# Optimization experiments

Measured on AMD Instinct MI355X. Metric: run time of the kernel, lower is better.

## Reference

```python
import jax, jax.numpy as jnp
import numpy as np

BLOCK_SIZE = 64
NUM_STEPS = 3
# pad_type='post', init_type='ones', attention_mask=None


def setup_inputs() -> dict:
    key = jax.random.key(0)
    k1, k2, k3 = jax.random.split(key, 3)
    B, H, S, D = 4, 16, 4096, 64
    return {
        "query": jax.random.normal(k1, (B, H, S, D), dtype=jnp.float32),
        "key": jax.random.normal(k2, (B, H, S, D), dtype=jnp.float32),
        "value": jax.random.normal(k3, (B, H, S, D), dtype=jnp.float32),
    }


def _soba_monarch(query, key, value):
    B, H, S, D = query.shape
    bs = BLOCK_SIZE
    nb = -(-S // bs)                 # ceil(S / bs)
    pad = nb * bs - S                # post padding amount
    q = query / (D ** 0.5)

    pad_cfg = ((0, 0), (0, 0), (0, pad), (0, 0))
    Qb = jnp.pad(q, pad_cfg).reshape(B, H, nb, bs, D)      # (l j) v -> l j v
    Kb = jnp.pad(key, pad_cfg).reshape(B, H, nb, bs, D)    # (k i) v -> k i v

    # validity of positions in the padded sequence (post-pad)
    pos_valid = (jnp.arange(nb * bs) < S).reshape(nb, bs)  # [block, within]
    # left factor shape (..., j, l, k): rows of the flattened (l j) axis
    left_mask = jnp.broadcast_to(pos_valid.T[:, :, None], (bs, nb, nb))      # j l k
    # right factor shape (..., k, j, i): columns of the flattened (k i) axis
    right_mask = jnp.broadcast_to(pos_valid[:, None, :], (nb, bs, bs))       # k j i

    NEG = jnp.finfo(q.dtype).min
    # init_type = 'ones'
    left = jnp.broadcast_to(
        jnp.where(left_mask, 1.0 / nb, 0.0), (B, H, bs, nb, nb)
    ).astype(q.dtype)

    for _ in range(NUM_STEPS):
        # beta[k,j,i] = sum_{l,v} left[j,l,k] Q[l,j,v] K[k,i,v]
        beta = jnp.einsum('bhjlk,bhljv,bhkiv->bhkji', left, Qb, Kb, optimize=True)
        tau = jnp.swapaxes(jnp.sum(left, axis=-2), -1, -2)[..., None]        # bhkj1
        tau_zero = jnp.isclose(tau, 0.0)
        tau_safe = jnp.where(tau_zero, 1.0, tau)
        logits_r = jnp.where(right_mask & ~tau_zero, beta / tau_safe, NEG)
        right = jax.nn.softmax(logits_r, axis=-1)
        right = jnp.where(right_mask, right, 0.0)

        # alpha[j,1,k] = sum_i right[k,j,i] log right[k,j,i]  (xlogy)
        r_safe = jnp.where(right > 0, right, 1.0)
        alpha = jnp.sum(right * jnp.log(r_safe), axis=-1)                    # bhkj
        alpha = jnp.swapaxes(alpha, -1, -2)[..., None, :]                    # bhj1k

        beta2 = jnp.einsum('bhkji,bhljv,bhkiv->bhjlk', right, Qb, Kb, optimize=True)
        left = jax.nn.softmax(jnp.where(left_mask, beta2 - alpha, NEG), axis=-1)
        left = jnp.where(left_mask, left, 0.0)

    # multiply: z = L (R V)
    Vb = jnp.pad(value, pad_cfg).reshape(B, H, nb, bs, D)                    # k i v
    Y = jnp.einsum('bhkji,bhkiv->bhkjv', right, Vb)
    Z = jnp.einsum('bhjlk,bhkjv->bhljv', left, Y)
    z = Z.reshape(B, H, nb * bs, D)
    return z[..., :S, :]


def reference(query, key, value):
    return _soba_monarch(query, key, value)
```

## Files before the change

### kernel.cpp

```cpp
#include <hip/hip_runtime.h>


namespace {

typedef __attribute__((ext_vector_type(8))) short short8v;
typedef __attribute__((ext_vector_type(4))) float f32x4;

constexpr int HEADS = 64;
constexpr size_t HEADQ = 262144;
constexpr size_t MATF  = (size_t)HEADS * 262144;

#define MFMA(ACC, A, B) ACC = __builtin_amdgcn_mfma_f32_16x16x32_bf16(A, B, ACC, 0, 0, 0)
#define LD8(arr, row, g8) (*(const short8v*)((arr) + (row) * 72 + (g8) * 8))

__device__ __forceinline__ float rmax16(float m) {
    m = fmaxf(m, __shfl_xor(m, 1));
    m = fmaxf(m, __shfl_xor(m, 2));
    m = fmaxf(m, __shfl_xor(m, 4));
    m = fmaxf(m, __shfl_xor(m, 8));
    return m;
}
__device__ __forceinline__ float rsum16(float s) {
    s += __shfl_xor(s, 1);
    s += __shfl_xor(s, 2);
    s += __shfl_xor(s, 4);
    s += __shfl_xor(s, 8);
    return s;
}

__device__ __forceinline__ void bfsplit(float x, ushort& h, ushort& l) {
    uint u = __float_as_uint(x);
    uint hi = (u + 0x7FFFu + ((u >> 16) & 1u)) & 0xFFFF0000u;
    h = (ushort)(hi >> 16);
    l = (ushort)(__float_as_uint(x - __uint_as_float(hi)) >> 16);
}
__device__ __forceinline__ uint packbf(float x) {
    uint u = __float_as_uint(x);
    uint hi = (u + 0x7FFFu + ((u >> 16) & 1u)) & 0xFFFF0000u;
    return hi | (__float_as_uint(x - __uint_as_float(hi)) >> 16);
}

struct Frag16 { short8v h0, h1, l0, l1; };

__device__ __forceinline__ Frag16 load_packed16(const uint* p) {
    Frag16 f;
    #pragma unroll
    for (int q = 0; q < 4; ++q) {
        uint4 a = *(const uint4*)(p + 4 * q);
        uint vv[4] = {a.x, a.y, a.z, a.w};
        #pragma unroll
        for (int e = 0; e < 4; ++e) {
            const int i = 4 * q + e;
            const ushort hh = (ushort)(vv[e] >> 16), ll = (ushort)(vv[e] & 0xFFFFu);
            if (i < 8) { f.h0[i] = (short)hh; f.l0[i] = (short)ll; }
            else       { f.h1[i - 8] = (short)hh; f.l1[i - 8] = (short)ll; }
        }
    }
    return f;
}
__device__ __forceinline__ Frag16 load_f32x16(const float* p, float s) {
    Frag16 f;
    #pragma unroll
    for (int q = 0; q < 4; ++q) {
        float4 a = *(const float4*)(p + 4 * q);
        float vv[4] = {a.x * s, a.y * s, a.z * s, a.w * s};
        #pragma unroll
        for (int e = 0; e < 4; ++e) {
            const int i = 4 * q + e;
            ushort hh, ll; bfsplit(vv[e], hh, ll);
            if (i < 8) { f.h0[i] = (short)hh; f.l0[i] = (short)ll; }
            else       { f.h1[i - 8] = (short)hh; f.l1[i - 8] = (short)ll; }
        }
    }
    return f;
}
__device__ __forceinline__ void store_rows(ushort* H, ushort* L, int r, int c0,
                                           const Frag16& f) {
    *(short8v*)(H + r * 72 + c0)     = f.h0;
    *(short8v*)(H + r * 72 + c0 + 8) = f.h1;
    *(short8v*)(L + r * 72 + c0)     = f.l0;
    *(short8v*)(L + r * 72 + c0 + 8) = f.l1;
}
__device__ __forceinline__ void scatter_tr(ushort* H, ushort* L, int r, int c0,
                                           const Frag16& f) {
    #pragma unroll
    for (int e = 0; e < 8; ++e) {
        H[(c0 + e) * 72 + r] = (ushort)f.h0[e];
        L[(c0 + e) * 72 + r] = (ushort)f.l0[e];
    }
    #pragma unroll
    for (int e = 0; e < 8; ++e) {
        H[(c0 + 8 + e) * 72 + r] = (ushort)f.h1[e];
        L[(c0 + 8 + e) * 72 + r] = (ushort)f.l1[e];
    }
}

__device__ __forceinline__ void flush_u32(const uint* OS, uint* g, int tid) {
    #pragma unroll
    for (int q = 0; q < 4; ++q) {
        const int off = tid * 4 + q * 1024;
        uint4 v = *(const uint4*)(OS + (off >> 6) * 68 + (off & 63));
        *(uint4*)(g + off) = v;
    }
}

__device__ __forceinline__ void mmstep(const ushort* AH, const ushort* AL,
                                       const ushort* BH, const ushort* BL,
                                       int w, int lo4, int hi4, f32x4 acc[4]) {
    #pragma unroll
    for (int ks = 0; ks < 2; ++ks) {
        short8v ah = LD8(AH, 16 * w + lo4, hi4 + 4 * ks);
        short8v al = LD8(AL, 16 * w + lo4, hi4 + 4 * ks);
        #pragma unroll
        for (int t = 0; t < 4; ++t) {
            short8v bh = LD8(BH, 16 * t + lo4, hi4 + 4 * ks);
            short8v bl = LD8(BL, 16 * t + lo4, hi4 + 4 * ks);
            MFMA(acc[t], ah, bh); MFMA(acc[t], ah, bl); MFMA(acc[t], al, bh);
        }
    }
}

__global__ void kmean_kernel(const float* __restrict__ Q, uint* __restrict__ M) {
    const int wg = blockIdx.x;
    const int h  = wg >> 6, j = wg & 63;
    const int v  = threadIdx.x;
    const float* base = Q + (size_t)h * HEADQ + (size_t)j * 64 + v;
    float acc = 0.f;
    #pragma unroll
    for (int l = 0; l < 64; ++l) acc += base[(size_t)l * 4096];
    M[(size_t)wg * 64 + v] = packbf(acc * (1.0f / 512.0f));
}

template<int FIRST, int LAST>
__global__ __launch_bounds__(256) void bc_kernel(
    const uint*  __restrict__ Gsrc,
    const float* __restrict__ Kmat,
    const float* __restrict__ Vmat,
    const float* __restrict__ tauIn,
    uint*  __restrict__ HmOut,
    float* __restrict__ alphaOut,
    uint*  __restrict__ Yout)
{
    __shared__ uint SM[9216];
    ushort* Ah = (ushort*)SM;        ushort* Al = Ah + 4608;
    ushort* Bh = (ushort*)(SM + 4608); ushort* Bl = Bh + 4608;
    uint* OS  = SM + 4608;
    uint* OS2 = SM;

    const int wg = blockIdx.x, h = wg >> 6, k = wg & 63;
    const int tid = threadIdx.x, r = tid & 63, c0 = (tid >> 6) << 4;

    {
        const uint* gp = FIRST ? (Gsrc + ((size_t)h * 64 + r) * 64 + c0)
                               : (Gsrc + ((size_t)h * 64 + r) * 4096 + (size_t)k * 64 + c0);
        Frag16 fg = load_packed16(gp);
        store_rows(Ah, Al, r, c0, fg);
    }
    Frag16 fk = load_f32x16(Kmat + (size_t)h * HEADQ + (size_t)k * 4096 + r * 64 + c0, 1.f);
    store_rows(Bh, Bl, r, c0, fk);
    Frag16 fv;
    if (LAST)
        fv = load_f32x16(Vmat + (size_t)h * HEADQ + (size_t)k * 4096 + r * 64 + c0, 1.f);

    const int w = tid >> 6, lo4 = tid & 15, hi4 = (tid >> 4) & 3;
    float tvv[4];
    #pragma unroll
    for (int rr = 0; rr < 4; ++rr)
        tvv[rr] = FIRST ? 1.f : tauIn[((size_t)h * 64 + k) * 64 + 16 * w + 4 * hi4 + rr];
    __syncthreads();

    f32x4 acc[4] = {};
    mmstep(Ah, Al, Bh, Bl, w, lo4, hi4, acc);
    __syncthreads();

    #pragma unroll
    for (int rr = 0; rr < 4; ++rr) {
        const int j = 16 * w + 4 * hi4 + rr;
        const bool tz = !(tvv[rr] > 1e-8f);
        const float tvi = tz ? 1.f : 1.f / tvv[rr];
        float lg[4];
        #pragma unroll
        for (int t = 0; t < 4; ++t) lg[t] = acc[t][rr] * tvi;
        float m = rmax16(fmaxf(fmaxf(lg[0], lg[1]), fmaxf(lg[2], lg[3])));
        float e[4], s = 0.f;
        #pragma unroll
        for (int t = 0; t < 4; ++t) { e[t] = __expf(lg[t] - m); s += e[t]; }
        s = rsum16(s);
        const float inv = 1.f / s;
        float ap = 0.f;
        #pragma unroll
        for (int t = 0; t < 4; ++t) {
            const float rv = tz ? (1.f / 64.f) : e[t] * inv;
            ap += (rv > 0.f) ? rv * __logf(rv) : 0.f;
            ushort hh, ll; bfsplit(rv, hh, ll);
            Ah[j * 72 + 16 * t + lo4] = hh;
            Al[j * 72 + 16 * t + lo4] = ll;
        }
        ap = rsum16(ap);
        if (lo4 == 0) alphaOut[((size_t)h * 64 + j) * 64 + k] = ap;
    }
    scatter_tr(Bh, Bl, r, c0, fk);
    __syncthreads();

    f32x4 acc2[4] = {};
    mmstep(Ah, Al, Bh, Bl, w, lo4, hi4, acc2);
    f32x4 acc3[4] = {};
    if (LAST) {
        __syncthreads();
        scatter_tr(Bh, Bl, r, c0, fv);
        __syncthreads();
        mmstep(Ah, Al, Bh, Bl, w, lo4, hi4, acc3);
    }
    __syncthreads();

    #pragma unroll
    for (int rr = 0; rr < 4; ++rr) {
        const int j = 16 * w + 4 * hi4 + rr;
        #pragma unroll
        for (int t = 0; t < 4; ++t) OS[j * 68 + 16 * t + lo4] = packbf(acc2[t][rr]);
    }
    if (LAST) {
        #pragma unroll
        for (int rr = 0; rr < 4; ++rr) {
            const int j = 16 * w + 4 * hi4 + rr;
            #pragma unroll
            for (int t = 0; t < 4; ++t) OS2[j * 68 + 16 * t + lo4] = packbf(acc3[t][rr]);
        }
    }
    __syncthreads();
    flush_u32(OS, HmOut + (size_t)wg * 4096, tid);
    if (LAST) flush_u32(OS2, Yout + (size_t)wg * 4096, tid);
}

template<int LAST>
__global__ __launch_bounds__(256) void da_kernel(
    const float* __restrict__ Q,
    const uint*  __restrict__ HmIn,
    const float* __restrict__ alphaIn,
    const uint*  __restrict__ Yin,
    uint*  __restrict__ Gout,
    float* __restrict__ tauOut,
    float* __restrict__ Zout)
{
    __shared__ uint SM[9216];
    ushort* Ah = (ushort*)SM;        ushort* Al = Ah + 4608;
    ushort* Bh = (ushort*)(SM + 4608); ushort* Bl = Bh + 4608;
    uint*  OSu = SM + 4608;
    float* OSf = (float*)(SM + 4608);

    const int wg = blockIdx.x, h = wg >> 6, j = wg & 63;
    const int tid = threadIdx.x, r = tid & 63, c0 = (tid >> 6) << 4;

    Frag16 fq = load_f32x16(Q + (size_t)h * HEADQ + (size_t)r * 4096 + (size_t)j * 64 + c0,
                            0.125f);
    store_rows(Ah, Al, r, c0, fq);
    {
        Frag16 fh = load_packed16(HmIn + ((size_t)h * 64 + r) * 4096 + (size_t)j * 64 + c0);
        store_rows(Bh, Bl, r, c0, fh);
    }
    Frag16 fy;
    if (LAST)
        fy = load_packed16(Yin + ((size_t)h * 64 + r) * 4096 + (size_t)j * 64 + c0);

    const int w = tid >> 6, lo4 = tid & 15, hi4 = (tid >> 4) & 3;
    float av[4];
    #pragma unroll
    for (int t = 0; t < 4; ++t)
        av[t] = alphaIn[((size_t)h * 64 + j) * 64 + 16 * t + lo4];
    __syncthreads();

    f32x4 acc[4] = {};
    mmstep(Ah, Al, Bh, Bl, w, lo4, hi4, acc);
    __syncthreads();

    #pragma unroll
    for (int rr = 0; rr < 4; ++rr) {
        const int l = 16 * w + 4 * hi4 + rr;
        float lg[4];
        #pragma unroll
        for (int t = 0; t < 4; ++t) lg[t] = acc[t][rr] - av[t];
        float m = rmax16(fmaxf(fmaxf(lg[0], lg[1]), fmaxf(lg[2], lg[3])));
        float e[4], s = 0.f;
        #pragma unroll
        for (int t = 0; t < 4; ++t) { e[t] = __expf(lg[t] - m); s += e[t]; }
        s = rsum16(s);
        const float inv = 1.f / s;
        #pragma unroll
        for (int t = 0; t < 4; ++t) {
            const float lv = e[t] * inv;
            ushort hh, ll; bfsplit(lv, hh, ll);
            if (!LAST) { Bh[(16 * t + lo4) * 72 + l] = hh; Bl[(16 * t + lo4) * 72 + l] = ll; }
            else       { Bh[l * 72 + 16 * t + lo4] = hh; Bl[l * 72 + 16 * t + lo4] = ll; }
        }
    }
    if (!LAST) scatter_tr(Ah, Al, r, c0, fq);
    else       scatter_tr(Ah, Al, r, c0, fy);
    __syncthreads();

    if (!LAST) {
        f32x4 acc2[4] = {};
        f32x4 tacc = {};
        short8v onesb;
        #pragma unroll
        for (int e2 = 0; e2 < 8; ++e2) onesb[e2] = (lo4 == 0) ? (short)0x3F80 : (short)0;
        #pragma unroll
        for (int ks = 0; ks < 2; ++ks) {
            short8v ah = LD8(Bh, 16 * w + lo4, hi4 + 4 * ks);
            short8v al = LD8(Bl, 16 * w + lo4, hi4 + 4 * ks);
            MFMA(tacc, ah, onesb); MFMA(tacc, al, onesb);
            #pragma unroll
            for (int t = 0; t < 4; ++t) {
                short8v bh = LD8(Ah, 16 * t + lo4, hi4 + 4 * ks);
                short8v bl = LD8(Al, 16 * t + lo4, hi4 + 4 * ks);
                MFMA(acc2[t], ah, bh); MFMA(acc2[t], ah, bl); MFMA(acc2[t], al, bh);
            }
        }
        __syncthreads();
        #pragma unroll
        for (int rr = 0; rr < 4; ++rr) {
            const int kq = 16 * w + 4 * hi4 + rr;
            if (lo4 == 0) tauOut[((size_t)h * 64 + kq) * 64 + j] = tacc[rr];
            #pragma unroll
            for (int t = 0; t < 4; ++t) OSu[kq * 68 + 16 * t + lo4] = packbf(acc2[t][rr]);
        }
        __syncthreads();
        flush_u32(OSu, Gout + (size_t)wg * 4096, tid);
    } else {
        f32x4 acc2[4] = {};
        #pragma unroll
        for (int ks = 0; ks < 2; ++ks) {
            short8v ah = LD8(Bh, 16 * w + lo4, hi4 + 4 * ks);
            short8v al = LD8(Bl, 16 * w + lo4, hi4 + 4 * ks);
            #pragma unroll
            for (int t = 0; t < 4; ++t) {
                short8v bh = LD8(Ah, 16 * t + lo4, hi4 + 4 * ks);
                short8v bl = LD8(Al, 16 * t + lo4, hi4 + 4 * ks);
                MFMA(acc2[t], ah, bh); MFMA(acc2[t], ah, bl); MFMA(acc2[t], al, bh);
            }
        }
        __syncthreads();
        #pragma unroll
        for (int rr = 0; rr < 4; ++rr) {
            const int l = 16 * w + 4 * hi4 + rr;
            #pragma unroll
            for (int t = 0; t < 4; ++t) OSf[l * 68 + 16 * t + lo4] = acc2[t][rr];
        }
        __syncthreads();
        #pragma unroll
        for (int q = 0; q < 4; ++q) {
            const int l = (tid >> 4) + 16 * q;
            const int v4 = (tid & 15) * 4;
            float4 vv = *(const float4*)(OSf + l * 68 + v4);
            *(float4*)(Zout + (size_t)h * HEADQ + (size_t)l * 4096 + (size_t)j * 64 + v4) = vv;
        }
    }
}

}

extern "C" void kernel_launch(void* const* d_in, const int* in_sizes, int n_in,
                              void* d_out, int out_size, void* d_ws, size_t ws_size,
                              hipStream_t stream) {
    const float* Q = (const float*)d_in[0];
    const float* K = (const float*)d_in[1];
    const float* V = (const float*)d_in[2];
    float* out = (float*)d_out;

    char* ws = (char*)d_ws;
    const size_t MB = 1024 * 1024;
    uint*  G   = (uint*)(ws);
    uint*  Hm  = (uint*)(ws + 64 * MB);
    uint*  M   = (uint*)(ws + 128 * MB);
    float* al  = (float*)(ws + 129 * MB);
    float* tau = (float*)(ws + 130 * MB);

    const bool bigws = ws_size >= (size_t)196 * MB;
    uint*  Ybuf = bigws ? (uint*)(ws + 131 * MB) : (uint*)out;
    float* Zdst = bigws ? out : (float*)G;

    dim3 blk(256), grid(HEADS * 64);

    kmean_kernel<<<dim3(HEADS * 64), dim3(64), 0, stream>>>(Q, M);
    bc_kernel<1, 0><<<grid, blk, 0, stream>>>(M, K, nullptr, nullptr, Hm, al, nullptr);
    da_kernel<0>   <<<grid, blk, 0, stream>>>(Q, Hm, al, nullptr, G, tau, nullptr);
    bc_kernel<0, 0><<<grid, blk, 0, stream>>>(G, K, nullptr, tau, Hm, al, nullptr);
    da_kernel<0>   <<<grid, blk, 0, stream>>>(Q, Hm, al, nullptr, G, tau, nullptr);
    bc_kernel<0, 1><<<grid, blk, 0, stream>>>(G, K, V, tau, Hm, al, Ybuf);
    da_kernel<1>   <<<grid, blk, 0, stream>>>(Q, Hm, al, Ybuf, nullptr, nullptr, Zdst);
    if (!bigws)
        hipMemcpyAsync(d_out, G, MATF * sizeof(float), hipMemcpyDeviceToDevice, stream);
}
```

Measured before the change: 305.5 us.

## Process four blocks per workgroup with register prefetch and fp32 intermediates

Measured after the change: 409.8 us. +34.1%, slower.

```diff
diff --git a/kernel.cpp b/kernel.cpp
--- a/kernel.cpp
+++ b/kernel.cpp
@@ -34,43 +34,27 @@
     h = (ushort)(hi >> 16);
     l = (ushort)(__float_as_uint(x - __uint_as_float(hi)) >> 16);
 }
-__device__ __forceinline__ uint packbf(float x) {
-    uint u = __float_as_uint(x);
-    uint hi = (u + 0x7FFFu + ((u >> 16) & 1u)) & 0xFFFF0000u;
-    return hi | (__float_as_uint(x - __uint_as_float(hi)) >> 16);
-}
-
+
+struct Raw16  { float4 a, b, c, d; };
 struct Frag16 { short8v h0, h1, l0, l1; };
 
-__device__ __forceinline__ Frag16 load_packed16(const uint* p) {
+__device__ __forceinline__ Raw16 raw_load(const float* p) {
+    Raw16 r;
+    r.a = *(const float4*)(p);
+    r.b = *(const float4*)(p + 4);
+    r.c = *(const float4*)(p + 8);
+    r.d = *(const float4*)(p + 12);
+    return r;
+}
+__device__ __forceinline__ Frag16 split16(const Raw16& r, float s) {
+    float v[16] = {r.a.x*s, r.a.y*s, r.a.z*s, r.a.w*s, r.b.x*s, r.b.y*s, r.b.z*s, r.b.w*s,
+                   r.c.x*s, r.c.y*s, r.c.z*s, r.c.w*s, r.d.x*s, r.d.y*s, r.d.z*s, r.d.w*s};
     Frag16 f;
     #pragma unroll
-    for (int q = 0; q < 4; ++q) {
-        uint4 a = *(const uint4*)(p + 4 * q);
-        uint vv[4] = {a.x, a.y, a.z, a.w};
-        #pragma unroll
-        for (int e = 0; e < 4; ++e) {
-            const int i = 4 * q + e;
-            const ushort hh = (ushort)(vv[e] >> 16), ll = (ushort)(vv[e] & 0xFFFFu);
-            if (i < 8) { f.h0[i] = (short)hh; f.l0[i] = (short)ll; }
-            else       { f.h1[i - 8] = (short)hh; f.l1[i - 8] = (short)ll; }
-        }
-    }
-    return f;
-}
-__device__ __forceinline__ Frag16 load_f32x16(const float* p, float s) {
-    Frag16 f;
-    #pragma unroll
-    for (int q = 0; q < 4; ++q) {
-        float4 a = *(const float4*)(p + 4 * q);
-        float vv[4] = {a.x * s, a.y * s, a.z * s, a.w * s};
-        #pragma unroll
-        for (int e = 0; e < 4; ++e) {
-            const int i = 4 * q + e;
-            ushort hh, ll; bfsplit(vv[e], hh, ll);
-            if (i < 8) { f.h0[i] = (short)hh; f.l0[i] = (short)ll; }
-            else       { f.h1[i - 8] = (short)hh; f.l1[i - 8] = (short)ll; }
-        }
+    for (int e = 0; e < 16; ++e) {
+        ushort hh, ll; bfsplit(v[e], hh, ll);
+        if (e < 8) { f.h0[e] = (short)hh; f.l0[e] = (short)ll; }
+        else       { f.h1[e - 8] = (short)hh; f.l1[e - 8] = (short)ll; }
     }
     return f;
 }
@@ -95,12 +79,12 @@
     }
 }
 
-__device__ __forceinline__ void flush_u32(const uint* OS, uint* g, int tid) {
+__device__ __forceinline__ void flush_f32(const float* OS, float* g, int tid) {
     #pragma unroll
     for (int q = 0; q < 4; ++q) {
         const int off = tid * 4 + q * 1024;
-        uint4 v = *(const uint4*)(OS + (off >> 6) * 68 + (off & 63));
-        *(uint4*)(g + off) = v;
+        float4 v = *(const float4*)(OS + (off >> 6) * 68 + (off & 63));
+        *(float4*)(g + off) = v;
     }
 }
 
@@ -120,239 +104,251 @@
     }
 }
 
-__global__ void kmean_kernel(const float* __restrict__ Q, uint* __restrict__ M) {
+__global__ __launch_bounds__(256) void kmean_kernel(const float* __restrict__ Q,
+                                                    float* __restrict__ M) {
     const int wg = blockIdx.x;
-    const int h  = wg >> 6, j = wg & 63;
-    const int v  = threadIdx.x;
+    const int h  = wg >> 4;
+    const int j  = ((wg & 15) << 2) + (threadIdx.x >> 6);
+    const int v  = threadIdx.x & 63;
     const float* base = Q + (size_t)h * HEADQ + (size_t)j * 64 + v;
     float acc = 0.f;
     #pragma unroll
     for (int l = 0; l < 64; ++l) acc += base[(size_t)l * 4096];
-    M[(size_t)wg * 64 + v] = packbf(acc * (1.0f / 512.0f));
+    M[((size_t)h * 64 + j) * 64 + v] = acc * (1.0f / 512.0f);
 }
 
 template<int FIRST, int LAST>
-__global__ __launch_bounds__(256) void bc_kernel(
-    const uint*  __restrict__ Gsrc,
+__global__ __launch_bounds__(256, 4) void bc_kernel(
+    const float* __restrict__ Gsrc,
     const float* __restrict__ Kmat,
     const float* __restrict__ Vmat,
     const float* __restrict__ tauIn,
-    uint*  __restrict__ HmOut,
+    float* __restrict__ HmOut,
     float* __restrict__ alphaOut,
-    uint*  __restrict__ Yout)
+    float* __restrict__ Yout)
 {
     __shared__ uint SM[9216];
-    ushort* Ah = (ushort*)SM;        ushort* Al = Ah + 4608;
+    ushort* Ah = (ushort*)SM;          ushort* Al = Ah + 4608;
     ushort* Bh = (ushort*)(SM + 4608); ushort* Bl = Bh + 4608;
-    uint* OS  = SM + 4608;
-    uint* OS2 = SM;
-
-    const int wg = blockIdx.x, h = wg >> 6, k = wg & 63;
+    float* OSB = (float*)(SM + 4608);
+    float* OSA = (float*)SM;
+
+    const int wg = blockIdx.x, h = wg >> 4, k0 = (wg & 15) << 2;
     const int tid = threadIdx.x, r = tid & 63, c0 = (tid >> 6) << 4;
-
-    {
-        const uint* gp = FIRST ? (Gsrc + ((size_t)h * 64 + r) * 64 + c0)
-                               : (Gsrc + ((size_t)h * 64 + r) * 4096 + (size_t)k * 64 + c0);
-        Frag16 fg = load_packed16(gp);
-        store_rows(Ah, Al, r, c0, fg);
-    }
-    Frag16 fk = load_f32x16(Kmat + (size_t)h * HEADQ + (size_t)k * 4096 + r * 64 + c0, 1.f);
-    store_rows(Bh, Bl, r, c0, fk);
-    Frag16 fv;
-    if (LAST)
-        fv = load_f32x16(Vmat + (size_t)h * HEADQ + (size_t)k * 4096 + r * 64 + c0, 1.f);
-
     const int w = tid >> 6, lo4 = tid & 15, hi4 = (tid >> 4) & 3;
-    float tvv[4];
-    #pragma unroll
-    for (int rr = 0; rr < 4; ++rr)
-        tvv[rr] = FIRST ? 1.f : tauIn[((size_t)h * 64 + k) * 64 + 16 * w + 4 * hi4 + rr];
-    __syncthreads();
-
-    f32x4 acc[4] = {};
-    mmstep(Ah, Al, Bh, Bl, w, lo4, hi4, acc);
-    __syncthreads();
-
-    #pragma unroll
-    for (int rr = 0; rr < 4; ++rr) {
-        const int j = 16 * w + 4 * hi4 + rr;
-        const bool tz = !(tvv[rr] > 1e-8f);
-        const float tvi = tz ? 1.f : 1.f / tvv[rr];
-        float lg[4];
-        #pragma unroll
-        for (int t = 0; t < 4; ++t) lg[t] = acc[t][rr] * tvi;
-        float m = rmax16(fmaxf(fmaxf(lg[0], lg[1]), fmaxf(lg[2], lg[3])));
-        float e[4], s = 0.f;
-        #pragma unroll
-        for (int t = 0; t < 4; ++t) { e[t] = __expf(lg[t] - m); s += e[t]; }
-        s = rsum16(s);
-        const float inv = 1.f / s;
-        float ap = 0.f;
-        #pragma unroll
-        for (int t = 0; t < 4; ++t) {
-            const float rv = tz ? (1.f / 64.f) : e[t] * inv;
-            ap += (rv > 0.f) ? rv * __logf(rv) : 0.f;
-            ushort hh, ll; bfsplit(rv, hh, ll);
-            Ah[j * 72 + 16 * t + lo4] = hh;
-            Al[j * 72 + 16 * t + lo4] = ll;
-        }
-        ap = rsum16(ap);
-        if (lo4 == 0) alphaOut[((size_t)h * 64 + j) * 64 + k] = ap;
-    }
-    scatter_tr(Bh, Bl, r, c0, fk);
-    __syncthreads();
-
-    f32x4 acc2[4] = {};
-    mmstep(Ah, Al, Bh, Bl, w, lo4, hi4, acc2);
-    f32x4 acc3[4] = {};
-    if (LAST) {
-        __syncthreads();
-        scatter_tr(Bh, Bl, r, c0, fv);
-        __syncthreads();
-        mmstep(Ah, Al, Bh, Bl, w, lo4, hi4, acc3);
-    }
-    __syncthreads();
-
-    #pragma unroll
-    for (int rr = 0; rr < 4; ++rr) {
-        const int j = 16 * w + 4 * hi4 + rr;
-        #pragma unroll
-        for (int t = 0; t < 4; ++t) OS[j * 68 + 16 * t + lo4] = packbf(acc2[t][rr]);
-    }
-    if (LAST) {
+
+    Raw16 nG = raw_load(FIRST ? Gsrc + ((size_t)h * 64 + r) * 64 + c0
+                              : Gsrc + ((size_t)h * 64 + r) * 4096 + (size_t)k0 * 64 + c0);
+    Raw16 nK = raw_load(Kmat + (size_t)h * HEADQ + (size_t)k0 * 4096 + r * 64 + c0);
+
+    for (int t = 0; t < 4; ++t) {
+        const int k = k0 + t;
+        float tvv[4];
+        #pragma unroll
+        for (int rr = 0; rr < 4; ++rr)
+            tvv[rr] = FIRST ? 1.f
+                : tauIn[((size_t)h * 64 + 16 * w + 4 * hi4 + rr) * 64 + k];
+
+        store_rows(Ah, Al, r, c0, split16(nG, 1.f));
+        Frag16 fk = split16(nK, 1.f);
+        store_rows(Bh, Bl, r, c0, fk);
+        Raw16 rawV;
+        if (LAST)
+            rawV = raw_load(Vmat + (size_t)h * HEADQ + (size_t)k * 4096 + r * 64 + c0);
+        if (t < 3) {
+            nG = raw_load(FIRST ? Gsrc + ((size_t)h * 64 + r) * 64 + c0
+                                : Gsrc + ((size_t)h * 64 + r) * 4096 + (size_t)(k + 1) * 64 + c0);
+            nK = raw_load(Kmat + (size_t)h * HEADQ + (size_t)(k + 1) * 4096 + r * 64 + c0);
+        }
+        __syncthreads();
+
+        f32x4 acc[4] = {};
+        mmstep(Ah, Al, Bh, Bl, w, lo4, hi4, acc);
+        __syncthreads();
+
         #pragma unroll
         for (int rr = 0; rr < 4; ++rr) {
             const int j = 16 * w + 4 * hi4 + rr;
-            #pragma unroll
-            for (int t = 0; t < 4; ++t) OS2[j * 68 + 16 * t + lo4] = packbf(acc3[t][rr]);
-        }
-    }
-    __syncthreads();
-    flush_u32(OS, HmOut + (size_t)wg * 4096, tid);
-    if (LAST) flush_u32(OS2, Yout + (size_t)wg * 4096, tid);
+            const bool tz = !(tvv[rr] > 1e-8f);
+            const float tvi = tz ? 1.f : 1.f / tvv[rr];
+            float lg[4];
+            #pragma unroll
+            for (int tt = 0; tt < 4; ++tt) lg[tt] = acc[tt][rr] * tvi;
+            float m = rmax16(fmaxf(fmaxf(lg[0], lg[1]), fmaxf(lg[2], lg[3])));
+            float e[4], s = 0.f;
+            #pragma unroll
+            for (int tt = 0; tt < 4; ++tt) { e[tt] = __expf(lg[tt] - m); s += e[tt]; }
+            s = rsum16(s);
+            const float inv = 1.f / s;
+            float ap = 0.f;
+            #pragma unroll
+            for (int tt = 0; tt < 4; ++tt) {
+                const float rv = tz ? (1.f / 64.f) : e[tt] * inv;
+                ap += (rv > 0.f) ? rv * __logf(rv) : 0.f;
+                ushort hh, ll; bfsplit(rv, hh, ll);
+                Ah[j * 72 + 16 * tt + lo4] = hh;
+                Al[j * 72 + 16 * tt + lo4] = ll;
+            }
+            ap = rsum16(ap);
+            if (lo4 == 0) alphaOut[((size_t)h * 64 + k) * 64 + j] = ap;
+        }
+        scatter_tr(Bh, Bl, r, c0, fk);
+        __syncthreads();
+
+        f32x4 acc2[4] = {};
+        mmstep(Ah, Al, Bh, Bl, w, lo4, hi4, acc2);
+        f32x4 acc3[4] = {};
+        if (LAST) {
+            __syncthreads();
+            scatter_tr(Bh, Bl, r, c0, split16(rawV, 1.f));
+            __syncthreads();
+            mmstep(Ah, Al, Bh, Bl, w, lo4, hi4, acc3);
+        }
+        __syncthreads();
+
+        #pragma unroll
+        for (int rr = 0; rr < 4; ++rr) {
+            const int j = 16 * w + 4 * hi4 + rr;
+            #pragma unroll
+            for (int tt = 0; tt < 4; ++tt) {
+                OSB[j * 68 + 16 * tt + lo4] = acc2[tt][rr];
+                if (LAST) OSA[j * 68 + 16 * tt + lo4] = acc3[tt][rr];
+            }
+        }
+        __syncthreads();
+        flush_f32(OSB, HmOut + ((size_t)h * 64 + k) * 4096, tid);
+        if (LAST) flush_f32(OSA, Yout + ((size_t)h * 64 + k) * 4096, tid);
+        __syncthreads();
+    }
 }
 
 template<int LAST>
-__global__ __launch_bounds__(256) void da_kernel(
+__global__ __launch_bounds__(256, 4) void da_kernel(
     const float* __restrict__ Q,
-    const uint*  __restrict__ HmIn,
+    const float* __restrict__ HmIn,
     const float* __restrict__ alphaIn,
-    const uint*  __restrict__ Yin,
-    uint*  __restrict__ Gout,
+    const float* __restrict__ Yin,
+    float* __restrict__ Gout,
     float* __restrict__ tauOut,
     float* __restrict__ Zout)
 {
     __shared__ uint SM[9216];
-    ushort* Ah = (ushort*)SM;        ushort* Al = Ah + 4608;
+    ushort* Ah = (ushort*)SM;          ushort* Al = Ah + 4608;
     ushort* Bh = (ushort*)(SM + 4608); ushort* Bl = Bh + 4608;
-    uint*  OSu = SM + 4608;
-    float* OSf = (float*)(SM + 4608);
-
-    const int wg = blockIdx.x, h = wg >> 6, j = wg & 63;
+    float* OSB = (float*)(SM + 4608);
+
+    const int wg = blockIdx.x, h = wg >> 4, j0 = (wg & 15) << 2;
     const int tid = threadIdx.x, r = tid & 63, c0 = (tid >> 6) << 4;
-
-    Frag16 fq = load_f32x16(Q + (size_t)h * HEADQ + (size_t)r * 4096 + (size_t)j * 64 + c0,
-                            0.125f);
-    store_rows(Ah, Al, r, c0, fq);
-    {
-        Frag16 fh = load_packed16(HmIn + ((size_t)h * 64 + r) * 4096 + (size_t)j * 64 + c0);
-        store_rows(Bh, Bl, r, c0, fh);
-    }
-    Frag16 fy;
-    if (LAST)
-        fy = load_packed16(Yin + ((size_t)h * 64 + r) * 4096 + (size_t)j * 64 + c0);
-
     const int w = tid >> 6, lo4 = tid & 15, hi4 = (tid >> 4) & 3;
-    float av[4];
-    #pragma unroll
-    for (int t = 0; t < 4; ++t)
-        av[t] = alphaIn[((size_t)h * 64 + j) * 64 + 16 * t + lo4];
-    __syncthreads();
-
-    f32x4 acc[4] = {};
-    mmstep(Ah, Al, Bh, Bl, w, lo4, hi4, acc);
-    __syncthreads();
-
-    #pragma unroll
-    for (int rr = 0; rr < 4; ++rr) {
-        const int l = 16 * w + 4 * hi4 + rr;
-        float lg[4];
-        #pragma unroll
-        for (int t = 0; t < 4; ++t) lg[t] = acc[t][rr] - av[t];
-        float m = rmax16(fmaxf(fmaxf(lg[0], lg[1]), fmaxf(lg[2], lg[3])));
-        float e[4], s = 0.f;
-        #pragma unroll
-        for (int t = 0; t < 4; ++t) { e[t] = __expf(lg[t] - m); s += e[t]; }
-        s = rsum16(s);
-        const float inv = 1.f / s;
-        #pragma unroll
-        for (int t = 0; t < 4; ++t) {
-            const float lv = e[t] * inv;
-            ushort hh, ll; bfsplit(lv, hh, ll);
-            if (!LAST) { Bh[(16 * t + lo4) * 72 + l] = hh; Bl[(16 * t + lo4) * 72 + l] = ll; }
-            else       { Bh[l * 72 + 16 * t + lo4] = hh; Bl[l * 72 + 16 * t + lo4] = ll; }
-        }
-    }
-    if (!LAST) scatter_tr(Ah, Al, r, c0, fq);
-    else       scatter_tr(Ah, Al, r, c0, fy);
-    __syncthreads();
-
-    if (!LAST) {
-        f32x4 acc2[4] = {};
-        f32x4 tacc = {};
-        short8v onesb;
-        #pragma unroll
-        for (int e2 = 0; e2 < 8; ++e2) onesb[e2] = (lo4 == 0) ? (short)0x3F80 : (short)0;
-        #pragma unroll
-        for (int ks = 0; ks < 2; ++ks) {
-            short8v ah = LD8(Bh, 16 * w + lo4, hi4 + 4 * ks);
-            short8v al = LD8(Bl, 16 * w + lo4, hi4 + 4 * ks);
-            MFMA(tacc, ah, onesb); MFMA(tacc, al, onesb);
-            #pragma unroll
-            for (int t = 0; t < 4; ++t) {
-                short8v bh = LD8(Ah, 16 * t + lo4, hi4 + 4 * ks);
-                short8v bl = LD8(Al, 16 * t + lo4, hi4 + 4 * ks);
-                MFMA(acc2[t], ah, bh); MFMA(acc2[t], ah, bl); MFMA(acc2[t], al, bh);
-            }
-        }
-        __syncthreads();
-        #pragma unroll
-        for (int rr = 0; rr < 4; ++rr) {
-            const int kq = 16 * w + 4 * hi4 + rr;
-            if (lo4 == 0) tauOut[((size_t)h * 64 + kq) * 64 + j] = tacc[rr];
-            #pragma unroll
-            for (int t = 0; t < 4; ++t) OSu[kq * 68 + 16 * t + lo4] = packbf(acc2[t][rr]);
-        }
-        __syncthreads();
-        flush_u32(OSu, Gout + (size_t)wg * 4096, tid);
-    } else {
-        f32x4 acc2[4] = {};
-        #pragma unroll
-        for (int ks = 0; ks < 2; ++ks) {
-            short8v ah = LD8(Bh, 16 * w + lo4, hi4 + 4 * ks);
-            short8v al = LD8(Bl, 16 * w + lo4, hi4 + 4 * ks);
-            #pragma unroll
-            for (int t = 0; t < 4; ++t) {
-                short8v bh = LD8(Ah, 16 * t + lo4, hi4 + 4 * ks);
-                short8v bl = LD8(Al, 16 * t + lo4, hi4 + 4 * ks);
-                MFMA(acc2[t], ah, bh); MFMA(acc2[t], ah, bl); MFMA(acc2[t], al, bh);
-            }
-        }
-        __syncthreads();
+
+    Raw16 nQ = raw_load(Q + (size_t)h * HEADQ + (size_t)r * 4096 + (size_t)j0 * 64 + c0);
+    Raw16 nH = raw_load(HmIn + ((size_t)h * 64 + r) * 4096 + (size_t)j0 * 64 + c0);
+
+    for (int t = 0; t < 4; ++t) {
+        const int j = j0 + t;
+        float av[4];
+        #pragma unroll
+        for (int tt = 0; tt < 4; ++tt)
+            av[tt] = alphaIn[((size_t)h * 64 + 16 * tt + lo4) * 64 + j];
+
+        Frag16 fq = split16(nQ, 0.125f);
+        store_rows(Ah, Al, r, c0, fq);
+        store_rows(Bh, Bl, r, c0, split16(nH, 1.f));
+        Raw16 rawY;
+        if (LAST)
+            rawY = raw_load(Yin + ((size_t)h * 64 + r) * 4096 + (size_t)j * 64 + c0);
+        if (t < 3) {
+            nQ = raw_load(Q + (size_t)h * HEADQ + (size_t)r * 4096 + (size_t)(j + 1) * 64 + c0);
+            nH = raw_load(HmIn + ((size_t)h * 64 + r) * 4096 + (size_t)(j + 1) * 64 + c0);
+        }
+        __syncthreads();
+
+        f32x4 acc[4] = {};
+        mmstep(Ah, Al, Bh, Bl, w, lo4, hi4, acc);
+        __syncthreads();
+
         #pragma unroll
         for (int rr = 0; rr < 4; ++rr) {
             const int l = 16 * w + 4 * hi4 + rr;
-            #pragma unroll
-            for (int t = 0; t < 4; ++t) OSf[l * 68 + 16 * t + lo4] = acc2[t][rr];
-        }
-        __syncthreads();
-        #pragma unroll
-        for (int q = 0; q < 4; ++q) {
-            const int l = (tid >> 4) + 16 * q;
-            const int v4 = (tid & 15) * 4;
-            float4 vv = *(const float4*)(OSf + l * 68 + v4);
-            *(float4*)(Zout + (size_t)h * HEADQ + (size_t)l * 4096 + (size_t)j * 64 + v4) = vv;
-        }
+            float lg[4];
+            #pragma unroll
+            for (int tt = 0; tt < 4; ++tt) lg[tt] = acc[tt][rr] - av[tt];
+            float m = rmax16(fmaxf(fmaxf(lg[0], lg[1]), fmaxf(lg[2], lg[3])));
+            float e[4], s = 0.f;
+            #pragma unroll
+            for (int tt = 0; tt < 4; ++tt) { e[tt] = __expf(lg[tt] - m); s += e[tt]; }
+            s = rsum16(s);
+            const float inv = 1.f / s;
+            #pragma unroll
+            for (int tt = 0; tt < 4; ++tt) {
+                const float lv = e[tt] * inv;
+                ushort hh, ll; bfsplit(lv, hh, ll);
+                if (!LAST) { Bh[(16 * tt + lo4) * 72 + l] = hh; Bl[(16 * tt + lo4) * 72 + l] = ll; }
+                else       { Bh[l * 72 + 16 * tt + lo4] = hh; Bl[l * 72 + 16 * tt + lo4] = ll; }
+            }
+        }
+        if (!LAST) scatter_tr(Ah, Al, r, c0, fq);
+        else       scatter_tr(Ah, Al, r, c0, split16(rawY, 1.f));
+        __syncthreads();
+
+        if (!LAST) {
+            f32x4 acc2[4] = {};
+            f32x4 tacc = {};
+            short8v onesb;
+            #pragma unroll
+            for (int e2 = 0; e2 < 8; ++e2) onesb[e2] = (lo4 == 0) ? (short)0x3F80 : (short)0;
+            #pragma unroll
+            for (int ks = 0; ks < 2; ++ks) {
+                short8v ah = LD8(Bh, 16 * w + lo4, hi4 + 4 * ks);
+                short8v al = LD8(Bl, 16 * w + lo4, hi4 + 4 * ks);
+                MFMA(tacc, ah, onesb); MFMA(tacc, al, onesb);
+                #pragma unroll
+                for (int tt = 0; tt < 4; ++tt) {
+                    short8v bh = LD8(Ah, 16 * tt + lo4, hi4 + 4 * ks);
+                    short8v bl = LD8(Al, 16 * tt + lo4, hi4 + 4 * ks);
+                    MFMA(acc2[tt], ah, bh); MFMA(acc2[tt], ah, bl); MFMA(acc2[tt], al, bh);
+                }
+            }
+            __syncthreads();
+            #pragma unroll
+            for (int rr = 0; rr < 4; ++rr) {
+                const int kq = 16 * w + 4 * hi4 + rr;
+                if (lo4 == 0) tauOut[((size_t)h * 64 + j) * 64 + kq] = tacc[rr];
+                #pragma unroll
+                for (int tt = 0; tt < 4; ++tt) OSB[kq * 68 + 16 * tt + lo4] = acc2[tt][rr];
+            }
+            __syncthreads();
+            flush_f32(OSB, Gout + ((size_t)h * 64 + j) * 4096, tid);
+        } else {
+            f32x4 acc2[4] = {};
+            #pragma unroll
+            for (int ks = 0; ks < 2; ++ks) {
+                short8v ah = LD8(Bh, 16 * w + lo4, hi4 + 4 * ks);
+                short8v al = LD8(Bl, 16 * w + lo4, hi4 + 4 * ks);
+                #pragma unroll
+                for (int tt = 0; tt < 4; ++tt) {
+                    short8v bh = LD8(Ah, 16 * tt + lo4, hi4 + 4 * ks);
+                    short8v bl = LD8(Al, 16 * tt + lo4, hi4 + 4 * ks);
+                    MFMA(acc2[tt], ah, bh); MFMA(acc2[tt], ah, bl); MFMA(acc2[tt], al, bh);
+                }
+            }
+            __syncthreads();
+            #pragma unroll
+            for (int rr = 0; rr < 4; ++rr) {
+                const int l = 16 * w + 4 * hi4 + rr;
+                #pragma unroll
+                for (int tt = 0; tt < 4; ++tt) OSB[l * 68 + 16 * tt + lo4] = acc2[tt][rr];
+            }
+            __syncthreads();
+            #pragma unroll
+            for (int q = 0; q < 4; ++q) {
+                const int l = (tid >> 4) + 16 * q;
+                const int v4 = (tid & 15) * 4;
+                float4 vv = *(const float4*)(OSB + l * 68 + v4);
+                *(float4*)(Zout + (size_t)h * HEADQ + (size_t)l * 4096 + (size_t)j * 64 + v4) = vv;
+            }
+        }
+        __syncthreads();
     }
 }
 
@@ -368,19 +364,19 @@
 
     char* ws = (char*)d_ws;
     const size_t MB = 1024 * 1024;
-    uint*  G   = (uint*)(ws);
-    uint*  Hm  = (uint*)(ws + 64 * MB);
-    uint*  M   = (uint*)(ws + 128 * MB);
+    float* G   = (float*)(ws);
+    float* Hm  = (float*)(ws + 64 * MB);
+    float* M   = (float*)(ws + 128 * MB);
     float* al  = (float*)(ws + 129 * MB);
     float* tau = (float*)(ws + 130 * MB);
 
     const bool bigws = ws_size >= (size_t)196 * MB;
-    uint*  Ybuf = bigws ? (uint*)(ws + 131 * MB) : (uint*)out;
-    float* Zdst = bigws ? out : (float*)G;
-
-    dim3 blk(256), grid(HEADS * 64);
-
-    kmean_kernel<<<dim3(HEADS * 64), dim3(64), 0, stream>>>(Q, M);
+    float* Ybuf = bigws ? (float*)(ws + 131 * MB) : out;
+    float* Zdst = bigws ? out : G;
+
+    dim3 blk(256), grid(1024);
+
+    kmean_kernel<<<grid, blk, 0, stream>>>(Q, M);
     bc_kernel<1, 0><<<grid, blk, 0, stream>>>(M, K, nullptr, nullptr, Hm, al, nullptr);
     da_kernel<0>   <<<grid, blk, 0, stream>>>(Q, Hm, al, nullptr, G, tau, nullptr);
     bc_kernel<0, 0><<<grid, blk, 0, stream>>>(G, K, nullptr, tau, Hm, al, nullptr);
```
